# Optimization experiments

Measured on AMD Instinct MI355X. Metric: run time of the kernel, lower is better.

## Reference

```python
import jax, jax.numpy as jnp
import numpy as np

B, T, HOR, N = 64, 12, 12, 1024
DIN, DOUT, YCOV, H, K, E = 1, 1, 1, 64, 3, 8


def setup_inputs() -> dict:
    key = jax.random.key(0)
    ks = jax.random.split(key, 10)
    def g(k, shape, s=1.0):
        return jax.random.normal(k, shape, dtype=jnp.float32) * s
    # xavier-ish scale for GCN weights: 1/sqrt(fan_in)
    gi = 1.0 / np.sqrt(K * (DIN + H))
    di = 1.0 / np.sqrt(K * (DOUT + YCOV + H))
    return {
        "x": jax.random.uniform(ks[0], (B, T, N, DIN), dtype=jnp.float32),
        "y_cov": jax.random.uniform(ks[1], (B, HOR, N, YCOV), dtype=jnp.float32),
        "node_emb": g(ks[2], (N, E), 1.0),
        "enc_gate_W": g(ks[3], (K * (DIN + H), 2 * H), gi),
        "enc_gate_b": jnp.zeros((2 * H,), jnp.float32),
        "enc_upd_W": g(ks[4], (K * (DIN + H), H), gi),
        "enc_upd_b": jnp.zeros((H,), jnp.float32),
        "dec_gate_W": g(ks[5], (K * (DOUT + YCOV + H), 2 * H), di),
        "dec_gate_b": jnp.zeros((2 * H,), jnp.float32),
        "dec_upd_W": g(ks[6], (K * (DOUT + YCOV + H), H), di),
        "dec_upd_b": jnp.zeros((H,), jnp.float32),
        "proj_W": g(ks[7], (H, DOUT), 1.0 / np.sqrt(H)),
        "proj_b": jnp.zeros((DOUT,), jnp.float32),
    }


def _cheb_supports(A):
    # support_set = [I, A, 2*A@A - I, ...], cheb_k terms
    s = [jnp.eye(A.shape[0], dtype=A.dtype), A]
    for _ in range(2, K):
        s.append(2.0 * A @ s[-1] - s[-2])
    return jnp.stack(s)  # [K, N, N]


def _gcn(x, sup, W, b):
    # x: [B,N,C]; sup: [K,N,N]; matches torch cat([s_k @ x], -1) ordering (k-major)
    bb, nn, cc = x.shape
    xg = jnp.einsum('knm,bmc->bnkc', sup, x).reshape(bb, nn, K * cc)
    return xg @ W + b


def _cell(x, h, sup, gW, gb, uW, ub):
    zr = jax.nn.sigmoid(_gcn(jnp.concatenate([x, h], -1), sup, gW, gb))
    z, r = jnp.split(zr, 2, axis=-1)
    hc = jnp.tanh(_gcn(jnp.concatenate([x, z * h], -1), sup, uW, ub))
    return r * h + (1.0 - r) * hc


def reference(x, y_cov, node_emb, enc_gate_W, enc_gate_b, enc_upd_W, enc_upd_b,
              dec_gate_W, dec_gate_b, dec_upd_W, dec_upd_b, proj_W, proj_b):
    # adaptive adjacency from node embeddings (AGCRN-style)
    A = jax.nn.softmax(jax.nn.relu(node_emb @ node_emb.T), axis=-1)
    sup = _cheb_supports(A)

    h0 = jnp.zeros((B, N, H), x.dtype)

    def enc_step(h, xt):
        h2 = _cell(xt, h, sup, enc_gate_W, enc_gate_b, enc_upd_W, enc_upd_b)
        return h2, None
    h_enc, _ = jax.lax.scan(enc_step, h0, jnp.swapaxes(x, 0, 1))  # final state [B,N,H]

    go0 = jnp.zeros((B, N, DOUT), x.dtype)

    def dec_step(carry, yt):
        h, go = carry
        h2 = _cell(jnp.concatenate([go, yt], -1), h, sup,
                   dec_gate_W, dec_gate_b, dec_upd_W, dec_upd_b)
        go2 = h2 @ proj_W + proj_b
        return (h2, go2), go2
    _, outs = jax.lax.scan(dec_step, (h_enc, go0), jnp.swapaxes(y_cov, 0, 1))
    return jnp.swapaxes(outs, 0, 1)  # [B, HOR, N, DOUT]
```

## Files before the change

kernel.cpp:

```cpp
#include <hip/hip_runtime.h>
#include <math.h>

constexpr int N = 1024, B = 64, T = 12, HOR = 12, H = 64, E = 8;
constexpr size_t NBH = 4194304;

constexpr size_t A_off   = 0;
constexpr size_t Pxy_off = 1048576;
constexpr size_t h_off   = Pxy_off + 3145728;
constexpr size_t Ph_off  = h_off + NBH;
constexpr size_t zh_off  = Ph_off + 2 * NBH;
constexpr size_t r_off   = zh_off + NBH;
constexpr size_t go_off  = r_off + NBH;
constexpr size_t A2_off  = go_off + 65536;
constexpr size_t Bth_off = A2_off + 1048576;
constexpr size_t Btz_off = Bth_off + 2162688;
constexpr size_t xyK_off = Btz_off + 2097152;
constexpr size_t Pgo_off = xyK_off + 786432;
constexpr size_t wp_off  = Pgo_off + 131072;

typedef __attribute__((ext_vector_type(8))) short short8;
typedef __attribute__((ext_vector_type(4))) float f32x4;

__device__ __forceinline__ unsigned f2bf(float x) {
  unsigned u = __float_as_uint(x);
  return (u + 0x7fffu + ((u >> 16) & 1u)) >> 16;
}
__device__ __forceinline__ float bf2f(unsigned h) {
  return __uint_as_float(h << 16);
}
__device__ __forceinline__ void split4(float4 v, uint2& hi, uint2& lo) {
  unsigned h0 = f2bf(v.x), h1 = f2bf(v.y), h2 = f2bf(v.z), h3 = f2bf(v.w);
  unsigned l0 = f2bf(v.x - bf2f(h0)), l1 = f2bf(v.y - bf2f(h1));
  unsigned l2 = f2bf(v.z - bf2f(h2)), l3 = f2bf(v.w - bf2f(h3));
  hi.x = (h0 & 0xffffu) | (h1 << 16); hi.y = (h2 & 0xffffu) | (h3 << 16);
  lo.x = (l0 & 0xffffu) | (l1 << 16); lo.y = (l2 & 0xffffu) | (l3 << 16);
}

typedef const __attribute__((address_space(1))) void gas_t;
typedef __attribute__((address_space(3))) void las_t;

__global__ __launch_bounds__(256) void build_A(const float* __restrict__ emb,
                                               float* __restrict__ A) {
  __shared__ float sE[N * E];
  __shared__ float sv[N];
  __shared__ float rmax[4], rsum[4];
  const int i = blockIdx.x;
  for (int idx = threadIdx.x; idx < N * E / 4; idx += 256)
    ((float4*)sE)[idx] = ((const float4*)emb)[idx];
  __syncthreads();
  float ei[E];
#pragma unroll
  for (int e = 0; e < E; ++e) ei[e] = sE[i * E + e];
  float mymax = 0.f;
  for (int j = threadIdx.x; j < N; j += 256) {
    float d = 0.f;
#pragma unroll
    for (int e = 0; e < E; ++e) d = fmaf(ei[e], sE[j * E + e], d);
    d = fmaxf(d, 0.f);
    sv[j] = d;
    mymax = fmaxf(mymax, d);
  }
  for (int off = 32; off; off >>= 1) mymax = fmaxf(mymax, __shfl_down(mymax, off));
  const int wid = threadIdx.x >> 6, lid = threadIdx.x & 63;
  if (lid == 0) rmax[wid] = mymax;
  __syncthreads();
  const float m = fmaxf(fmaxf(rmax[0], rmax[1]), fmaxf(rmax[2], rmax[3]));
  float mysum = 0.f;
  for (int j = threadIdx.x; j < N; j += 256) {
    float ev = expf(sv[j] - m);
    sv[j] = ev;
    mysum += ev;
  }
  for (int off = 32; off; off >>= 1) mysum += __shfl_down(mysum, off);
  if (lid == 0) rsum[wid] = mysum;
  __syncthreads();
  const float inv = 1.f / (rsum[0] + rsum[1] + rsum[2] + rsum[3]);
  for (int j = threadIdx.x; j < N; j += 256) A[i * N + j] = sv[j] * inv;
}

__global__ __launch_bounds__(256) void pack_split_S(const float* __restrict__ A,
                                                    ushort* __restrict__ L,
                                                    ushort* __restrict__ R) {
  __shared__ float tile[32][33];
  const int bx = blockIdx.x * 32;
  const int by = blockIdx.y * 32;
  const int tx = threadIdx.x & 31;
  const int tg = threadIdx.x >> 5;
#pragma unroll
  for (int p = 0; p < 4; ++p) {
    int ty = tg * 4 + p;
    tile[ty][tx] = A[(size_t)(by + ty) * 1024 + bx + tx];
  }
  __syncthreads();
#pragma unroll
  for (int p = 0; p < 4; ++p) {
    int ty = tg * 4 + p;
    float v = tile[ty][tx];
    unsigned h = f2bf(v);
    unsigned l = f2bf(v - bf2f(h));
    size_t lb = (size_t)(by + ty) * 3072 + 3 * (bx + tx);
    L[lb + 0] = (ushort)h; L[lb + 1] = (ushort)l; L[lb + 2] = (ushort)h;
    float w = tile[tx][ty];
    unsigned hh = f2bf(w);
    unsigned ll = f2bf(w - bf2f(hh));
    size_t rbi = (size_t)(bx + ty) * 3072 + 3 * (by + tx);
    R[rbi + 0] = (ushort)hh; R[rbi + 1] = (ushort)hh; R[rbi + 2] = (ushort)ll;
  }
}

__global__ __launch_bounds__(256) void conv_bf16(const float* __restrict__ src,
                                                 ushort* __restrict__ dst) {
  int i = blockIdx.x * 256 + threadIdx.x;
  float4 v = ((const float4*)src)[i];
  ushort4 o;
  o.x = (ushort)f2bf(v.x); o.y = (ushort)f2bf(v.y);
  o.z = (ushort)f2bf(v.z); o.w = (ushort)f2bf(v.w);
  ((ushort4*)dst)[i] = o;
}

__global__ __launch_bounds__(256) void conv_xyK(const float* __restrict__ src,
                                                ushort* __restrict__ dst, int off) {
  int id = blockIdx.x * 256 + threadIdx.x;
  int tb = id >> 10, n = id & 1023;
  int tt = tb >> 6, b = tb & 63;
  dst[(size_t)(off + tb) * 1024 + n] = (ushort)f2bf(src[((size_t)b * T + tt) * 1024 + n]);
}

__global__ __launch_bounds__(256) void pack_W(const float* __restrict__ W,
                                              ushort* __restrict__ out,
                                              int CIN, int NC, int xoff) {
  int idx = blockIdx.x * 256 + threadIdx.x;
  int total = 3 * 2 * NC * 32;
  if (idx >= total) return;
  int kk = idx & 31;
  int colrest = idx >> 5;
  int col = colrest % NC;
  int rest = colrest / NC;
  int half = rest & 1;
  int s = rest >> 1;
  float v = W[(size_t)(s * CIN + xoff + half * 32 + kk) * NC + col];
  unsigned hi = f2bf(v);
  unsigned lo = f2bf(v - bf2f(hi));
  size_t base = (size_t)((s * 2 + half) * 2) * NC * 32;
  out[base + (size_t)col * 32 + kk] = (ushort)hi;
  out[base + (size_t)NC * 32 + (size_t)col * 32 + kk] = (ushort)lo;
}

__global__ __launch_bounds__(256) void gemm_s2p(
    const ushort* __restrict__ L, const ushort* __restrict__ R,
    float* __restrict__ P) {
  __shared__ ushort As[128 * 32];
  __shared__ ushort Bs[128 * 32];
  const int t = threadIdx.x;
  const int wave = t >> 6, lane = t & 63;
  const int bm = blockIdx.y * 128, bn = blockIdx.x * 128;
  const int wm = (wave & 1) * 64, wn = (wave >> 1) * 64;
  float* Pz = P + (size_t)blockIdx.z * 1048576;
  const int kbase = blockIdx.z * 768;

  const ushort* aSrc[2]; const ushort* bSrc[2];
  ushort* aDst[2]; ushort* bDst[2];
#pragma unroll
  for (int u = 0; u < 2; ++u) {
    int idx = wave * 128 + u * 64 + lane;
    int row = idx >> 2;
    int kq = (idx & 3) * 8;
    aSrc[u] = L + (size_t)(bm + row) * 3072 + kq;
    bSrc[u] = R + (size_t)(bn + row) * 3072 + kq;
    aDst[u] = &As[(wave * 128 + u * 64) * 8];
    bDst[u] = &Bs[(wave * 128 + u * 64) * 8];
  }
  const int lr = lane & 15;
  const int lk = (lane >> 4) * 8;
  f32x4 acc[4][4];
#pragma unroll
  for (int i = 0; i < 4; ++i)
#pragma unroll
    for (int j = 0; j < 4; ++j) acc[i][j] = {0.f, 0.f, 0.f, 0.f};

  for (int k0 = kbase; k0 < kbase + 768; k0 += 32) {
#pragma unroll
    for (int u = 0; u < 2; ++u) {
      __builtin_amdgcn_global_load_lds((gas_t*)(aSrc[u] + k0), (las_t*)aDst[u], 16, 0, 0);
      __builtin_amdgcn_global_load_lds((gas_t*)(bSrc[u] + k0), (las_t*)bDst[u], 16, 0, 0);
    }
    __syncthreads();
    short8 a[4], b[4];
#pragma unroll
    for (int i = 0; i < 4; ++i) a[i] = *(const short8*)&As[(wm + i * 16 + lr) * 32 + lk];
#pragma unroll
    for (int j = 0; j < 4; ++j) b[j] = *(const short8*)&Bs[(wn + j * 16 + lr) * 32 + lk];
#pragma unroll
    for (int i = 0; i < 4; ++i)
#pragma unroll
      for (int j = 0; j < 4; ++j)
        acc[i][j] = __builtin_amdgcn_mfma_f32_16x16x32_bf16(a[i], b[j], acc[i][j], 0, 0, 0);
    __syncthreads();
  }
  const int cr = (lane >> 4) * 4;
  const int cc = lane & 15;
#pragma unroll
  for (int i = 0; i < 4; ++i)
#pragma unroll
    for (int j = 0; j < 4; ++j) {
      int gm = bm + wm + i * 16 + cr;
      int gn = bn + wn + j * 16 + cc;
#pragma unroll
      for (int r = 0; r < 4; ++r)
        Pz[(size_t)(gm + r) * 1024 + gn] = acc[i][j][r];
    }
}

__global__ __launch_bounds__(256) void comb_s2(const float* __restrict__ P,
                                               ushort* __restrict__ A2) {
  int idx = blockIdx.x * 256 + threadIdx.x;
  float4 a = ((const float4*)P)[idx];
  float4 b = ((const float4*)(P + 1048576))[idx];
  float4 c = ((const float4*)(P + 2097152))[idx];
  float4 d = ((const float4*)(P + 3145728))[idx];
  int base = idx << 2;
  int m = base >> 10, c0 = base & 1023;
  float v0 = 2.f * (a.x + b.x + c.x + d.x) - (m == c0 + 0 ? 1.f : 0.f);
  float v1 = 2.f * (a.y + b.y + c.y + d.y) - (m == c0 + 1 ? 1.f : 0.f);
  float v2 = 2.f * (a.z + b.z + c.z + d.z) - (m == c0 + 2 ? 1.f : 0.f);
  float v3 = 2.f * (a.w + b.w + c.w + d.w) - (m == c0 + 3 ? 1.f : 0.f);
  ushort4 o;
  o.x = (ushort)f2bf(v0); o.y = (ushort)f2bf(v1);
  o.z = (ushort)f2bf(v2); o.w = (ushort)f2bf(v3);
  ((ushort4*)(A2 + 1048576))[idx] = o;
}

template <int CMODE>
__global__ __launch_bounds__(256) void gemm_bt(
    const ushort* __restrict__ A2, const ushort* __restrict__ Bt, int n1,
    float* __restrict__ C1, float* __restrict__ C2) {
  __shared__ ushort As[2][128 * 32];
  __shared__ ushort Bs[2][128 * 32];
  const int t = threadIdx.x;
  const int wave = t >> 6, lane = t & 63;
  const int bm = blockIdx.y * 128, bn = blockIdx.x * 128;
  const int wm = (wave & 1) * 64, wn = (wave >> 1) * 64;

  const ushort* aSrc[2]; const ushort* bSrc[2];
  ushort* aDst[2][2]; ushort* bDst[2][2];
#pragma unroll
  for (int u = 0; u < 2; ++u) {
    int idx = wave * 128 + u * 64 + lane;
    int row = idx >> 2;
    int kq = (idx & 3) * 8;
    aSrc[u] = A2 + (size_t)(bm + row) * 1024 + kq;
    bSrc[u] = Bt + (size_t)(bn + row) * 1024 + kq;
#pragma unroll
    for (int p = 0; p < 2; ++p) {
      aDst[p][u] = &As[p][(wave * 128 + u * 64) * 8];
      bDst[p][u] = &Bs[p][(wave * 128 + u * 64) * 8];
    }
  }
  const int lr = lane & 15, lk = (lane >> 4) * 8;
  int aOff[4], bOff[4];
#pragma unroll
  for (int i = 0; i < 4; ++i) {
    aOff[i] = (wm + i * 16 + lr) * 32 + lk;
    bOff[i] = (wn + i * 16 + lr) * 32 + lk;
  }
  f32x4 acc[4][4];
#pragma unroll
  for (int i = 0; i < 4; ++i)
#pragma unroll
    for (int j = 0; j < 4; ++j) acc[i][j] = {0.f, 0.f, 0.f, 0.f};

  for (int k0 = 0; k0 < 1024; k0 += 64) {
#pragma unroll
    for (int p = 0; p < 2; ++p)
#pragma unroll
      for (int u = 0; u < 2; ++u) {
        __builtin_amdgcn_global_load_lds((gas_t*)(aSrc[u] + k0 + p * 32),
                                         (las_t*)aDst[p][u], 16, 0, 0);
        __builtin_amdgcn_global_load_lds((gas_t*)(bSrc[u] + k0 + p * 32),
                                         (las_t*)bDst[p][u], 16, 0, 0);
      }
    __syncthreads();
#pragma unroll
    for (int p = 0; p < 2; ++p) {
      short8 a[4], b[4];
#pragma unroll
      for (int i = 0; i < 4; ++i) a[i] = *(const short8*)&As[p][aOff[i]];
#pragma unroll
      for (int j = 0; j < 4; ++j) b[j] = *(const short8*)&Bs[p][bOff[j]];
#pragma unroll
      for (int i = 0; i < 4; ++i)
#pragma unroll
        for (int j = 0; j < 4; ++j)
          acc[i][j] = __builtin_amdgcn_mfma_f32_16x16x32_bf16(a[i], b[j], acc[i][j], 0, 0, 0);
    }
    __syncthreads();
  }

  const int cr = (lane >> 4) * 4;
  const int cc = lane & 15;
#pragma unroll
  for (int i = 0; i < 4; ++i) {
#pragma unroll
    for (int j = 0; j < 4; ++j) {
      int gm = bm + wm + i * 16 + cr;
      int gn = bn + wn + j * 16 + cc;
      if (gn < n1) {
        if (CMODE == 0) {
          float* p = C1 + (size_t)gm * n1 + gn;
#pragma unroll
          for (int r = 0; r < 4; ++r) p[(size_t)r * n1] = acc[i][j][r];
        } else {
          int half = gm >> 10, nn = gm & 1023;
          float* p = C1 + (size_t)half * NBH +
                     ((size_t)(gn >> 6) * 1024 + nn) * 64 + (gn & 63);
#pragma unroll
          for (int r = 0; r < 4; ++r) p[(size_t)r * 64] = acc[i][j][r];
        }
      } else if (C2 != nullptr && gn < n1 + 64) {
        float* p = C2 + (size_t)gm * 64 + (gn - n1);
#pragma unroll
        for (int r = 0; r < 4; ++r) p[(size_t)r * 64] = acc[i][j][r];
      }
    }
  }
}

template <int NX>
__global__ __launch_bounds__(256, 4) void gate_mfma(
    const float* __restrict__ hmat, const float* __restrict__ Ph,
    const ushort* __restrict__ Wp, const float* __restrict__ Wf, const float* __restrict__ bias,
    const float* __restrict__ xb0, int xbs0, const float* __restrict__ xp0, int xs0,
    const float* __restrict__ xb1, int xbs1, const float* __restrict__ xp1, int xs1,
    float* __restrict__ zh, float* __restrict__ rbuf, ushort* __restrict__ Btz) {
  constexpr int CIN = NX + 64;
  __shared__ ushort smem[12288];
  ushort* Ah = smem;
  ushort* Al = smem + 2048;
  ushort* Bh = smem + 4096;
  ushort* Bl = smem + 8192;
  ushort* transT = smem;
  __shared__ float sxv[3][2][64];
  __shared__ float sWx[3][2][128];
  const int t = threadIdx.x;
  const int wave = t >> 6, lane = t & 63;
  const int bm = blockIdx.x * 64;
  const int wm = (wave & 1) * 32, wn = (wave >> 1) * 64;
  const int lr = lane & 15, lk = (lane >> 4) * 8;
  const float* srcs[3] = {hmat, Ph, Ph + NBH};

  if (t < 64) {
    int grow = bm + t;
    int n = grow & 1023, b = grow >> 10;
    sxv[0][0][t] = xb0[(size_t)b * xbs0 + n];
    sxv[1][0][t] = xp0[(size_t)n * xs0 + b];
    sxv[2][0][t] = xp0[(size_t)1024 * xs0 + (size_t)n * xs0 + b];
    if (NX == 2) {
      sxv[0][1][t] = xb1[(size_t)b * xbs1 + n];
      sxv[1][1][t] = xp1[(size_t)n * xs1 + b];
      sxv[2][1][t] = xp1[(size_t)1024 * xs1 + (size_t)n * xs1 + b];
    }
  } else if (t < 192) {
    int col = t - 64;
#pragma unroll
    for (int s = 0; s < 3; ++s)
#pragma unroll
      for (int f = 0; f < NX; ++f)
        sWx[s][f][col] = Wf[(size_t)(s * CIN + f) * 128 + col];
  }

  int arow[2], ajq[2];
#pragma unroll
  for (int p = 0; p < 2; ++p) {
    int f = p * 256 + t;
    arow[p] = f >> 3;
    ajq[p] = (f & 7) * 4;
  }
  float4 pf[2];
#pragma unroll
  for (int p = 0; p < 2; ++p)
    pf[p] = *(const float4*)(hmat + (size_t)(bm + arow[p]) * 64 + ajq[p]);

  f32x4 acc[2][4];
#pragma unroll
  for (int i = 0; i < 2; ++i)
#pragma unroll
    for (int j = 0; j < 4; ++j) acc[i][j] = {0.f, 0.f, 0.f, 0.f};

  for (int it = 0; it < 6; ++it) {
    const int s = it >> 1, half = it & 1;
#pragma unroll
    for (int p = 0; p < 2; ++p) {
      uint2 hi, lo;
      split4(pf[p], hi, lo);
      *(uint2*)&Ah[arow[p] * 32 + ajq[p]] = hi;
      *(uint2*)&Al[arow[p] * 32 + ajq[p]] = lo;
    }
    const ushort* wph = Wp + (size_t)((s * 2 + half) * 2) * (128 * 32);
    const ushort* wpl = wph + 128 * 32;
#pragma unroll
    for (int u = 0; u < 2; ++u) {
      int idx = wave * 128 + u * 64 + lane;
      __builtin_amdgcn_global_load_lds((gas_t*)(wph + idx * 8), (las_t*)&Bh[idx * 8], 16, 0, 0);
      __builtin_amdgcn_global_load_lds((gas_t*)(wpl + idx * 8), (las_t*)&Bl[idx * 8], 16, 0, 0);
    }
    __syncthreads();
    if (it < 5) {
      const float* nsrc = srcs[(it + 1) >> 1];
      const int nj0 = ((it + 1) & 1) * 32;
#pragma unroll
      for (int p = 0; p < 2; ++p)
        pf[p] = *(const float4*)(nsrc + (size_t)(bm + arow[p]) * 64 + nj0 + ajq[p]);
    }
    short8 ah[2], al[2], bh[4], bl[4];
#pragma unroll
    for (int i = 0; i < 2; ++i) {
      ah[i] = *(const short8*)&Ah[(wm + i * 16 + lr) * 32 + lk];
      al[i] = *(const short8*)&Al[(wm + i * 16 + lr) * 32 + lk];
    }
#pragma unroll
    for (int j = 0; j < 4; ++j) {
      bh[j] = *(const short8*)&Bh[(wn + j * 16 + lr) * 32 + lk];
      bl[j] = *(const short8*)&Bl[(wn + j * 16 + lr) * 32 + lk];
    }
#pragma unroll
    for (int i = 0; i < 2; ++i)
#pragma unroll
      for (int j = 0; j < 4; ++j) {
        acc[i][j] = __builtin_amdgcn_mfma_f32_16x16x32_bf16(ah[i], bh[j], acc[i][j], 0, 0, 0);
        acc[i][j] = __builtin_amdgcn_mfma_f32_16x16x32_bf16(al[i], bh[j], acc[i][j], 0, 0, 0);
        acc[i][j] = __builtin_amdgcn_mfma_f32_16x16x32_bf16(ah[i], bl[j], acc[i][j], 0, 0, 0);
      }
    __syncthreads();
  }

  const int cr = (lane >> 4) * 4;
  const int cc = lane & 15;
#pragma unroll
  for (int i = 0; i < 2; ++i) {
#pragma unroll
    for (int j = 0; j < 4; ++j) {
      int col = wn + j * 16 + cc;
      float bcol = bias[col];
#pragma unroll
      for (int r = 0; r < 4; ++r) {
        int rowl = wm + i * 16 + cr + r;
        int grow = bm + rowl;
        float v = acc[i][j][r] + bcol;
#pragma unroll
        for (int s = 0; s < 3; ++s)
#pragma unroll
          for (int f = 0; f < NX; ++f)
            v = fmaf(sxv[s][f][rowl], sWx[s][f][col], v);
        float sig = 1.f / (1.f + expf(-v));
        if (col < 64) {
          float zv = sig * hmat[(size_t)grow * 64 + col];
          zh[(size_t)grow * 64 + col] = zv;
          transT[col * 72 + rowl] = (ushort)f2bf(zv);
        } else {
          rbuf[(size_t)grow * 64 + col - 64] = sig;
        }
      }
    }
  }
  __syncthreads();
  const int bq = bm >> 10, nb = bm & 1023;
  for (int idx = t; idx < 512; idx += 256) {
    int j = idx >> 3, ch = idx & 7;
    uint4 v = *(const uint4*)&transT[j * 72 + ch * 8];
    *(uint4*)(Btz + (((size_t)(bq * 64 + j)) << 10) + nb + ch * 8) = v;
  }
}

template <int NX, int PROJ>
__global__ __launch_bounds__(256, 4) void upd_mfma(
    float* __restrict__ hmat, const float* __restrict__ zhb, const float* __restrict__ Pzh,
    const ushort* __restrict__ Wp, const float* __restrict__ Wf, const float* __restrict__ bias,
    const float* __restrict__ xb0, int xbs0, const float* __restrict__ xp0, int xs0,
    const float* __restrict__ xb1, int xbs1, const float* __restrict__ xp1, int xs1,
    const float* __restrict__ rbuf, ushort* __restrict__ Bth,
    const float* __restrict__ pW, const float* __restrict__ pb,
    float* __restrict__ gobuf, float* __restrict__ outp, int tstep) {
  constexpr int CIN = NX + 64;
  __shared__ ushort smem[8192];
  ushort* Ah = smem;
  ushort* Al = smem + 2048;
  ushort* Bh = smem + 4096;
  ushort* Bl = smem + 6144;
  ushort* transT = smem;
  __shared__ float sxv[3][2][64];
  __shared__ float sWx[3][2][64];
  __shared__ float part[2][64];
  const int t = threadIdx.x;
  const int wave = t >> 6, lane = t & 63;
  const int bm = blockIdx.x * 64;
  const int wm = (wave & 1) * 32, wn = (wave >> 1) * 32;
  const int lr = lane & 15, lk = (lane >> 4) * 8;
  const float* srcs[3] = {zhb, Pzh, Pzh + NBH};

  if (t < 64) {
    int grow = bm + t;
    int n = grow & 1023, b = grow >> 10;
    sxv[0][0][t] = xb0[(size_t)b * xbs0 + n];
    sxv[1][0][t] = xp0[(size_t)n * xs0 + b];
    sxv[2][0][t] = xp0[(size_t)1024 * xs0 + (size_t)n * xs0 + b];
    if (NX == 2) {
      sxv[0][1][t] = xb1[(size_t)b * xbs1 + n];
      sxv[1][1][t] = xp1[(size_t)n * xs1 + b];
      sxv[2][1][t] = xp1[(size_t)1024 * xs1 + (size_t)n * xs1 + b];
    }
  } else if (t < 128) {
    int col = t - 64;
#pragma unroll
    for (int s = 0; s < 3; ++s)
#pragma unroll
      for (int f = 0; f < NX; ++f)
        sWx[s][f][col] = Wf[(size_t)(s * CIN + f) * 64 + col];
  }

  int arow[2], ajq[2];
#pragma unroll
  for (int p = 0; p < 2; ++p) {
    int f = p * 256 + t;
    arow[p] = f >> 3;
    ajq[p] = (f & 7) * 4;
  }
  float4 pf[2];
#pragma unroll
  for (int p = 0; p < 2; ++p)
    pf[p] = *(const float4*)(zhb + (size_t)(bm + arow[p]) * 64 + ajq[p]);

  f32x4 acc[2][2];
#pragma unroll
  for (int i = 0; i < 2; ++i)
#pragma unroll
    for (int j = 0; j < 2; ++j) acc[i][j] = {0.f, 0.f, 0.f, 0.f};

  for (int it = 0; it < 6; ++it) {
    const int s = it >> 1, half = it & 1;
#pragma unroll
    for (int p = 0; p < 2; ++p) {
      uint2 hi, lo;
      split4(pf[p], hi, lo);
      *(uint2*)&Ah[arow[p] * 32 + ajq[p]] = hi;
      *(uint2*)&Al[arow[p] * 32 + ajq[p]] = lo;
    }
    const ushort* wph = Wp + (size_t)((s * 2 + half) * 2) * (64 * 32);
    const ushort* wpl = wph + 64 * 32;
    {
      int idx = wave * 64 + lane;
      __builtin_amdgcn_global_load_lds((gas_t*)(wph + idx * 8), (las_t*)&Bh[idx * 8], 16, 0, 0);
      __builtin_amdgcn_global_load_lds((gas_t*)(wpl + idx * 8), (las_t*)&Bl[idx * 8], 16, 0, 0);
    }
    __syncthreads();
    if (it < 5) {
      const float* nsrc = srcs[(it + 1) >> 1];
      const int nj0 = ((it + 1) & 1) * 32;
#pragma unroll
      for (int p = 0; p < 2; ++p)
        pf[p] = *(const float4*)(nsrc + (size_t)(bm + arow[p]) * 64 + nj0 + ajq[p]);
    }
    short8 ah[2], al[2], bh[2], bl[2];
#pragma unroll
    for (int i = 0; i < 2; ++i) {
      ah[i] = *(const short8*)&Ah[(wm + i * 16 + lr) * 32 + lk];
      al[i] = *(const short8*)&Al[(wm + i * 16 + lr) * 32 + lk];
    }
#pragma unroll
    for (int j = 0; j < 2; ++j) {
      bh[j] = *(const short8*)&Bh[(wn + j * 16 + lr) * 32 + lk];
      bl[j] = *(const short8*)&Bl[(wn + j * 16 + lr) * 32 + lk];
    }
#pragma unroll
    for (int i = 0; i < 2; ++i)
#pragma unroll
      for (int j = 0; j < 2; ++j) {
        acc[i][j] = __builtin_amdgcn_mfma_f32_16x16x32_bf16(ah[i], bh[j], acc[i][j], 0, 0, 0);
        acc[i][j] = __builtin_amdgcn_mfma_f32_16x16x32_bf16(al[i], bh[j], acc[i][j], 0, 0, 0);
        acc[i][j] = __builtin_amdgcn_mfma_f32_16x16x32_bf16(ah[i], bl[j], acc[i][j], 0, 0, 0);
      }
    __syncthreads();
  }

  const int cr = (lane >> 4) * 4;
  const int cc = lane & 15;
  float psv[2][4];
#pragma unroll
  for (int i = 0; i < 2; ++i)
#pragma unroll
    for (int r = 0; r < 4; ++r) psv[i][r] = 0.f;

#pragma unroll
  for (int i = 0; i < 2; ++i) {
#pragma unroll
    for (int j = 0; j < 2; ++j) {
      int col = wn + j * 16 + cc;
      float bcol = bias[col];
      float pwc = PROJ ? pW[col] : 0.f;
#pragma unroll
      for (int r = 0; r < 4; ++r) {
        int rowl = wm + i * 16 + cr + r;
        int grow = bm + rowl;
        float v = acc[i][j][r] + bcol;
#pragma unroll
        for (int s = 0; s < 3; ++s)
#pragma unroll
          for (int f = 0; f < NX; ++f)
            v = fmaf(sxv[s][f][rowl], sWx[s][f][col], v);
        float hc = tanhf(v);
        size_t idx = (size_t)grow * 64 + col;
        float rr = rbuf[idx];
        float ho = hmat[idx];
        float o = rr * ho + (1.f - rr) * hc;
        hmat[idx] = o;
        transT[col * 72 + rowl] = (ushort)f2bf(o);
        if (PROJ) psv[i][r] += o * pwc;
      }
    }
  }
  if (PROJ) {
#pragma unroll
    for (int i = 0; i < 2; ++i)
#pragma unroll
      for (int r = 0; r < 4; ++r)
#pragma unroll
        for (int off = 8; off; off >>= 1)
          psv[i][r] += __shfl_down(psv[i][r], off, 16);
    if (cc == 0) {
#pragma unroll
      for (int i = 0; i < 2; ++i)
#pragma unroll
        for (int r = 0; r < 4; ++r)
          part[wn >> 5][wm + i * 16 + cr + r] = psv[i][r];
    }
  }
  __syncthreads();
  const int bq = bm >> 10, nb = bm & 1023;
  for (int idx = t; idx < 512; idx += 256) {
    int j = idx >> 3, ch = idx & 7;
    uint4 v = *(const uint4*)&transT[j * 72 + ch * 8];
    *(uint4*)(Bth + (((size_t)(bq * 64 + j)) << 10) + nb + ch * 8) = v;
  }
  if (PROJ && t < 64) {
    int grow = bm + t;
    int n = grow & 1023, b = grow >> 10;
    float g = part[0][t] + part[1][t] + pb[0];
    gobuf[grow] = g;
    outp[((size_t)b * HOR + tstep) * N + n] = g;
    Bth[((size_t)(4096 + b)) * 1024 + n] = (ushort)f2bf(g);
  }
}

extern "C" void kernel_launch(void* const* d_in, const int* in_sizes, int n_in,
                              void* d_out, int out_size, void* d_ws, size_t ws_size,
                              hipStream_t stream) {
  const float* x    = (const float*)d_in[0];
  const float* ycov = (const float*)d_in[1];
  const float* emb  = (const float*)d_in[2];
  const float* egW  = (const float*)d_in[3];
  const float* egb  = (const float*)d_in[4];
  const float* euW  = (const float*)d_in[5];
  const float* eub  = (const float*)d_in[6];
  const float* dgW  = (const float*)d_in[7];
  const float* dgb  = (const float*)d_in[8];
  const float* duW  = (const float*)d_in[9];
  const float* dub  = (const float*)d_in[10];
  const float* pW   = (const float*)d_in[11];
  const float* pb   = (const float*)d_in[12];
  float* out = (float*)d_out;
  float* ws  = (float*)d_ws;

  float* Amat = ws + A_off;
  float* Pxy  = ws + Pxy_off;
  float* hmat = ws + h_off;
  float* Ph   = ws + Ph_off;
  float* zh   = ws + zh_off;
  float* rb   = ws + r_off;
  float* gob  = ws + go_off;
  float* Pgo  = ws + Pgo_off;
  ushort* A2   = (ushort*)(ws + A2_off);
  ushort* Bth  = (ushort*)(ws + Bth_off);
  ushort* Btz  = (ushort*)(ws + Btz_off);
  ushort* xyK  = (ushort*)(ws + xyK_off);
  ushort* AspL = (ushort*)(ws + zh_off);
  ushort* AspR = (ushort*)(ws + r_off);
  float*  Pp   = ws + Ph_off;
  ushort* WPge = (ushort*)(ws + wp_off);
  ushort* WPgd = WPge + 2 * 24576;
  ushort* WPue = WPgd + 2 * 24576;
  ushort* WPud = WPue + 2 * 12288;

  build_A<<<N, 256, 0, stream>>>(emb, Amat);
  pack_split_S<<<dim3(32, 32), 256, 0, stream>>>(Amat, AspL, AspR);
  gemm_s2p<<<dim3(8, 8, 4), 256, 0, stream>>>(AspL, AspR, Pp);
  comb_s2<<<1024, 256, 0, stream>>>(Pp, A2);
  conv_bf16<<<1024, 256, 0, stream>>>(Amat, A2);
  conv_xyK<<<3072, 256, 0, stream>>>(x, xyK, 0);
  conv_xyK<<<3072, 256, 0, stream>>>(ycov, xyK, 768);
  pack_W<<<(3 * 2 * 128 * 32 + 255) / 256, 256, 0, stream>>>(egW, WPge, 65, 128, 1);
  pack_W<<<(3 * 2 * 128 * 32 + 255) / 256, 256, 0, stream>>>(dgW, WPgd, 66, 128, 2);
  pack_W<<<(3 * 2 * 64 * 32 + 255) / 256, 256, 0, stream>>>(euW, WPue, 65, 64, 1);
  pack_W<<<(3 * 2 * 64 * 32 + 255) / 256, 256, 0, stream>>>(duW, WPud, 66, 64, 2);
  gemm_bt<0><<<dim3(12, 16), 256, 0, stream>>>(A2, xyK, 1536, Pxy, nullptr);
  (void)hipMemsetAsync(hmat, 0, NBH * sizeof(float), stream);
  (void)hipMemsetAsync(Ph, 0, 2 * NBH * sizeof(float), stream);
  (void)hipMemsetAsync(gob, 0, 65536 * sizeof(float), stream);
  (void)hipMemsetAsync(Bth + (size_t)4096 * 1024, 0, 128 * 1024 * sizeof(ushort), stream);

  for (int t = 0; t < T; ++t) {
    if (t > 0)
      gemm_bt<1><<<dim3(32, 16), 256, 0, stream>>>(A2, Bth, 4096, Ph, nullptr);
    gate_mfma<1><<<1024, 256, 0, stream>>>(hmat, Ph, WPge, egW, egb,
                                           x + t * 1024, T * 1024, Pxy + t * 64, 1536,
                                           nullptr, 0, nullptr, 0, zh, rb, Btz);
    if (t > 0)
      gemm_bt<1><<<dim3(32, 16), 256, 0, stream>>>(A2, Btz, 4096, Ph, nullptr);
    upd_mfma<1, 0><<<1024, 256, 0, stream>>>(hmat, zh, Ph, WPue, euW, eub,
                                             x + t * 1024, T * 1024, Pxy + t * 64, 1536,
                                             nullptr, 0, nullptr, 0, rb, Bth,
                                             nullptr, nullptr, nullptr, nullptr, 0);
  }

  for (int t = 0; t < HOR; ++t) {
    gemm_bt<1><<<dim3(33, 16), 256, 0, stream>>>(A2, Bth, 4096, Ph, Pgo);
    gate_mfma<2><<<1024, 256, 0, stream>>>(hmat, Ph, WPgd, dgW, dgb,
                                           gob, 1024, Pgo, 64,
                                           ycov + t * 1024, HOR * 1024,
                                           Pxy + 768 + t * 64, 1536, zh, rb, Btz);
    gemm_bt<1><<<dim3(32, 16), 256, 0, stream>>>(A2, Btz, 4096, Ph, nullptr);
    upd_mfma<2, 1><<<1024, 256, 0, stream>>>(hmat, zh, Ph, WPud, duW, dub,
                                             gob, 1024, Pgo, 64,
                                             ycov + t * 1024, HOR * 1024,
                                             Pxy + 768 + t * 64, 1536,
                                             rb, Bth, pW, pb, gob, out, t);
  }
}
```

Baseline: 2.701 ms.

## Store graph-propagated hidden states in fp16 and use single fp16 MFMA

The support-times-hidden GEMM now writes its outputs (Ph) as fp16 instead of fp32. The gate and update kernels consume them with one fp16 MFMA per tile instead of the bf16 hi/lo split, which needed three MFMAs plus on-the-fly splitting. The identity term (hmat/zh) keeps the split-bf16 path, and weights for supports 1-2 are packed separately into fp16. This halves traffic for the largest intermediate buffers and cuts MFMA work. The gemm_bt grid is also flattened and remapped into grouped tiles for better L2 locality, at the cost of some precision on the propagated terms.

```diff
diff --git a/kernel.cpp b/kernel.cpp
--- a/kernel.cpp
+++ b/kernel.cpp
@@ -19,6 +19,7 @@
 constexpr size_t wp_off  = Pgo_off + 131072;
 
 typedef __attribute__((ext_vector_type(8))) short short8;
+typedef _Float16 half8 __attribute__((ext_vector_type(8)));
 typedef __attribute__((ext_vector_type(4))) float f32x4;
 
 __device__ __forceinline__ unsigned f2bf(float x) {
@@ -27,6 +28,12 @@
 }
 __device__ __forceinline__ float bf2f(unsigned h) {
   return __uint_as_float(h << 16);
+}
+__device__ __forceinline__ ushort f2h(float x) {
+  _Float16 h = (_Float16)x;
+  ushort u;
+  __builtin_memcpy(&u, &h, 2);
+  return u;
 }
 __device__ __forceinline__ void split4(float4 v, uint2& hi, uint2& lo) {
   unsigned h0 = f2bf(v.x), h1 = f2bf(v.y), h2 = f2bf(v.z), h3 = f2bf(v.w);
@@ -126,24 +133,39 @@
   dst[(size_t)(off + tb) * 1024 + n] = (ushort)f2bf(src[((size_t)b * T + tt) * 1024 + n]);
 }
 
-__global__ __launch_bounds__(256) void pack_W(const float* __restrict__ W,
-                                              ushort* __restrict__ out,
-                                              int CIN, int NC, int xoff) {
+__global__ __launch_bounds__(256) void pack_Wbf(const float* __restrict__ W,
+                                                ushort* __restrict__ out,
+                                                int CIN, int NC, int xoff) {
   int idx = blockIdx.x * 256 + threadIdx.x;
-  int total = 3 * 2 * NC * 32;
+  int total = 2 * NC * 32;
   if (idx >= total) return;
   int kk = idx & 31;
-  int colrest = idx >> 5;
-  int col = colrest % NC;
-  int rest = colrest / NC;
-  int half = rest & 1;
-  int s = rest >> 1;
-  float v = W[(size_t)(s * CIN + xoff + half * 32 + kk) * NC + col];
+  int rest = idx >> 5;
+  int col = rest % NC;
+  int half = rest / NC;
+  float v = W[(size_t)(xoff + half * 32 + kk) * NC + col];
   unsigned hi = f2bf(v);
   unsigned lo = f2bf(v - bf2f(hi));
-  size_t base = (size_t)((s * 2 + half) * 2) * NC * 32;
+  size_t base = (size_t)(half * 2) * NC * 32;
   out[base + (size_t)col * 32 + kk] = (ushort)hi;
   out[base + (size_t)NC * 32 + (size_t)col * 32 + kk] = (ushort)lo;
+}
+
+__global__ __launch_bounds__(256) void pack_W16(const float* __restrict__ W,
+                                                ushort* __restrict__ out,
+                                                int CIN, int NC, int xoff) {
+  int idx = blockIdx.x * 256 + threadIdx.x;
+  int total = 2 * 2 * NC * 32;
+  if (idx >= total) return;
+  int kk = idx & 31;
+  int rest = idx >> 5;
+  int col = rest % NC;
+  rest /= NC;
+  int half = rest & 1;
+  int s1 = rest >> 1;
+  int s = s1 + 1;
+  float v = W[(size_t)(s * CIN + xoff + half * 32 + kk) * NC + col];
+  out[(size_t)(s1 * 2 + half) * NC * 32 + (size_t)col * 32 + kk] = f2h(v);
 }
 
 __global__ __launch_bounds__(256) void gemm_s2p(
@@ -233,12 +255,24 @@
 template <int CMODE>
 __global__ __launch_bounds__(256) void gemm_bt(
     const ushort* __restrict__ A2, const ushort* __restrict__ Bt, int n1,
-    float* __restrict__ C1, float* __restrict__ C2) {
+    ushort* __restrict__ C1h, float* __restrict__ C1f, float* __restrict__ C2) {
   __shared__ ushort As[2][128 * 32];
   __shared__ ushort Bs[2][128 * 32];
   const int t = threadIdx.x;
   const int wave = t >> 6, lane = t & 63;
-  const int bm = blockIdx.y * 128, bn = blockIdx.x * 128;
+  int bxi, byi;
+  if (CMODE == 0) {
+    bxi = blockIdx.x; byi = blockIdx.y;
+  } else {
+    int lin = blockIdx.x;
+    if (lin < 512) {
+      bxi = (lin & 7) * 4 + ((lin >> 3) & 3);
+      byi = lin >> 5;
+    } else {
+      bxi = 32; byi = lin - 512;
+    }
+  }
+  const int bm = byi * 128, bn = bxi * 128;
   const int wm = (wave & 1) * 64, wn = (wave >> 1) * 64;
 
   const ushort* aSrc[2]; const ushort* bSrc[2];
@@ -306,15 +340,15 @@
       int gn = bn + wn + j * 16 + cc;
       if (gn < n1) {
         if (CMODE == 0) {
-          float* p = C1 + (size_t)gm * n1 + gn;
+          float* p = C1f + (size_t)gm * n1 + gn;
 #pragma unroll
           for (int r = 0; r < 4; ++r) p[(size_t)r * n1] = acc[i][j][r];
         } else {
           int half = gm >> 10, nn = gm & 1023;
-          float* p = C1 + (size_t)half * NBH +
-                     ((size_t)(gn >> 6) * 1024 + nn) * 64 + (gn & 63);
-#pragma unroll
-          for (int r = 0; r < 4; ++r) p[(size_t)r * 64] = acc[i][j][r];
+          ushort* p = C1h + (size_t)half * NBH +
+                      ((size_t)(gn >> 6) * 1024 + nn) * 64 + (gn & 63);
+#pragma unroll
+          for (int r = 0; r < 4; ++r) p[(size_t)r * 64] = f2h(acc[i][j][r]);
         }
       } else if (C2 != nullptr && gn < n1 + 64) {
         float* p = C2 + (size_t)gm * 64 + (gn - n1);
@@ -327,8 +361,9 @@
 
 template <int NX>
 __global__ __launch_bounds__(256, 4) void gate_mfma(
-    const float* __restrict__ hmat, const float* __restrict__ Ph,
-    const ushort* __restrict__ Wp, const float* __restrict__ Wf, const float* __restrict__ bias,
+    const float* __restrict__ hmat, const ushort* __restrict__ Ph16,
+    const ushort* __restrict__ Wbf, const ushort* __restrict__ W16,
+    const float* __restrict__ Wf, const float* __restrict__ bias,
     const float* __restrict__ xb0, int xbs0, const float* __restrict__ xp0, int xs0,
     const float* __restrict__ xb1, int xbs1, const float* __restrict__ xp1, int xs1,
     float* __restrict__ zh, float* __restrict__ rbuf, ushort* __restrict__ Btz) {
@@ -338,6 +373,8 @@
   ushort* Al = smem + 2048;
   ushort* Bh = smem + 4096;
   ushort* Bl = smem + 8192;
+  ushort* A16 = smem;
+  ushort* B16 = smem + 4096;
   ushort* transT = smem;
   __shared__ float sxv[3][2][64];
   __shared__ float sWx[3][2][128];
@@ -346,7 +383,6 @@
   const int bm = blockIdx.x * 64;
   const int wm = (wave & 1) * 32, wn = (wave >> 1) * 64;
   const int lr = lane & 15, lk = (lane >> 4) * 8;
-  const float* srcs[3] = {hmat, Ph, Ph + NBH};
 
   if (t < 64) {
     int grow = bm + t;
@@ -375,10 +411,13 @@
     arow[p] = f >> 3;
     ajq[p] = (f & 7) * 4;
   }
+  const int hrow = t >> 2, hjq = (t & 3) * 8;
+
   float4 pf[2];
 #pragma unroll
   for (int p = 0; p < 2; ++p)
     pf[p] = *(const float4*)(hmat + (size_t)(bm + arow[p]) * 64 + ajq[p]);
+  uint4 px;
 
   f32x4 acc[2][4];
 #pragma unroll
@@ -386,8 +425,8 @@
 #pragma unroll
     for (int j = 0; j < 4; ++j) acc[i][j] = {0.f, 0.f, 0.f, 0.f};
 
-  for (int it = 0; it < 6; ++it) {
-    const int s = it >> 1, half = it & 1;
+#pragma unroll
+  for (int half = 0; half < 2; ++half) {
 #pragma unroll
     for (int p = 0; p < 2; ++p) {
       uint2 hi, lo;
@@ -395,7 +434,7 @@
       *(uint2*)&Ah[arow[p] * 32 + ajq[p]] = hi;
       *(uint2*)&Al[arow[p] * 32 + ajq[p]] = lo;
     }
-    const ushort* wph = Wp + (size_t)((s * 2 + half) * 2) * (128 * 32);
+    const ushort* wph = Wbf + (size_t)(half * 2) * (128 * 32);
     const ushort* wpl = wph + 128 * 32;
 #pragma unroll
     for (int u = 0; u < 2; ++u) {
@@ -404,12 +443,12 @@
       __builtin_amdgcn_global_load_lds((gas_t*)(wpl + idx * 8), (las_t*)&Bl[idx * 8], 16, 0, 0);
     }
     __syncthreads();
-    if (it < 5) {
-      const float* nsrc = srcs[(it + 1) >> 1];
-      const int nj0 = ((it + 1) & 1) * 32;
+    if (half == 0) {
 #pragma unroll
       for (int p = 0; p < 2; ++p)
-        pf[p] = *(const float4*)(nsrc + (size_t)(bm + arow[p]) * 64 + nj0 + ajq[p]);
+        pf[p] = *(const float4*)(hmat + (size_t)(bm + arow[p]) * 64 + 32 + ajq[p]);
+    } else {
+      px = *(const uint4*)(Ph16 + (size_t)(bm + hrow) * 64 + hjq);
     }
     short8 ah[2], al[2], bh[4], bl[4];
 #pragma unroll
@@ -430,6 +469,36 @@
         acc[i][j] = __builtin_amdgcn_mfma_f32_16x16x32_bf16(al[i], bh[j], acc[i][j], 0, 0, 0);
         acc[i][j] = __builtin_amdgcn_mfma_f32_16x16x32_bf16(ah[i], bl[j], acc[i][j], 0, 0, 0);
       }
+    __syncthreads();
+  }
+
+  for (int it = 0; it < 4; ++it) {
+    const int s1 = it >> 1, half = it & 1;
+    *(uint4*)&A16[hrow * 32 + hjq] = px;
+    const ushort* w16 = W16 + (size_t)(s1 * 2 + half) * (128 * 32);
+#pragma unroll
+    for (int u = 0; u < 2; ++u) {
+      int idx = wave * 128 + u * 64 + lane;
+      __builtin_amdgcn_global_load_lds((gas_t*)(w16 + idx * 8), (las_t*)&B16[idx * 8], 16, 0, 0);
+    }
+    __syncthreads();
+    if (it < 3) {
+      const int nit = it + 1;
+      const ushort* src = Ph16 + (size_t)(nit >> 1) * NBH;
+      px = *(const uint4*)(src + (size_t)(bm + hrow) * 64 + (nit & 1) * 32 + hjq);
+    }
+    half8 a16[2], b16[4];
+#pragma unroll
+    for (int i = 0; i < 2; ++i)
+      a16[i] = *(const half8*)&A16[(wm + i * 16 + lr) * 32 + lk];
+#pragma unroll
+    for (int j = 0; j < 4; ++j)
+      b16[j] = *(const half8*)&B16[(wn + j * 16 + lr) * 32 + lk];
+#pragma unroll
+    for (int i = 0; i < 2; ++i)
+#pragma unroll
+      for (int j = 0; j < 4; ++j)
+        acc[i][j] = __builtin_amdgcn_mfma_f32_16x16x32_f16(a16[i], b16[j], acc[i][j], 0, 0, 0);
     __syncthreads();
   }
 
@@ -473,8 +542,9 @@
 
 template <int NX, int PROJ>
 __global__ __launch_bounds__(256, 4) void upd_mfma(
-    float* __restrict__ hmat, const float* __restrict__ zhb, const float* __restrict__ Pzh,
-    const ushort* __restrict__ Wp, const float* __restrict__ Wf, const float* __restrict__ bias,
+    float* __restrict__ hmat, const float* __restrict__ zhb, const ushort* __restrict__ Pzh16,
+    const ushort* __restrict__ Wbf, const ushort* __restrict__ W16,
+    const float* __restrict__ Wf, const float* __restrict__ bias,
     const float* __restrict__ xb0, int xbs0, const float* __restrict__ xp0, int xs0,
     const float* __restrict__ xb1, int xbs1, const float* __restrict__ xp1, int xs1,
     const float* __restrict__ rbuf, ushort* __restrict__ Bth,
@@ -486,6 +556,8 @@
   ushort* Al = smem + 2048;
   ushort* Bh = smem + 4096;
   ushort* Bl = smem + 6144;
+  ushort* A16 = smem;
+  ushort* B16 = smem + 4096;
   ushort* transT = smem;
   __shared__ float sxv[3][2][64];
   __shared__ float sWx[3][2][64];
@@ -495,7 +567,6 @@
   const int bm = blockIdx.x * 64;
   const int wm = (wave & 1) * 32, wn = (wave >> 1) * 32;
   const int lr = lane & 15, lk = (lane >> 4) * 8;
-  const float* srcs[3] = {zhb, Pzh, Pzh + NBH};
 
   if (t < 64) {
     int grow = bm + t;
@@ -524,10 +595,13 @@
     arow[p] = f >> 3;
     ajq[p] = (f & 7) * 4;
   }
+  const int hrow = t >> 2, hjq = (t & 3) * 8;
+
   float4 pf[2];
 #pragma unroll
   for (int p = 0; p < 2; ++p)
     pf[p] = *(const float4*)(zhb + (size_t)(bm + arow[p]) * 64 + ajq[p]);
+  uint4 px;
 
   f32x4 acc[2][2];
 #pragma unroll
@@ -535,8 +609,8 @@
 #pragma unroll
     for (int j = 0; j < 2; ++j) acc[i][j] = {0.f, 0.f, 0.f, 0.f};
 
-  for (int it = 0; it < 6; ++it) {
-    const int s = it >> 1, half = it & 1;
+#pragma unroll
+  for (int half = 0; half < 2; ++half) {
 #pragma unroll
     for (int p = 0; p < 2; ++p) {
       uint2 hi, lo;
@@ -544,7 +618,7 @@
       *(uint2*)&Ah[arow[p] * 32 + ajq[p]] = hi;
       *(uint2*)&Al[arow[p] * 32 + ajq[p]] = lo;
     }
-    const ushort* wph = Wp + (size_t)((s * 2 + half) * 2) * (64 * 32);
+    const ushort* wph = Wbf + (size_t)(half * 2) * (64 * 32);
     const ushort* wpl = wph + 64 * 32;
     {
       int idx = wave * 64 + lane;
@@ -552,12 +626,12 @@
       __builtin_amdgcn_global_load_lds((gas_t*)(wpl + idx * 8), (las_t*)&Bl[idx * 8], 16, 0, 0);
     }
     __syncthreads();
-    if (it < 5) {
-      const float* nsrc = srcs[(it + 1) >> 1];
-      const int nj0 = ((it + 1) & 1) * 32;
+    if (half == 0) {
 #pragma unroll
       for (int p = 0; p < 2; ++p)
-        pf[p] = *(const float4*)(nsrc + (size_t)(bm + arow[p]) * 64 + nj0 + ajq[p]);
+        pf[p] = *(const float4*)(zhb + (size_t)(bm + arow[p]) * 64 + 32 + ajq[p]);
+    } else {
+      px = *(const uint4*)(Pzh16 + (size_t)(bm + hrow) * 64 + hjq);
     }
     short8 ah[2], al[2], bh[2], bl[2];
 #pragma unroll
@@ -578,6 +652,35 @@
         acc[i][j] = __builtin_amdgcn_mfma_f32_16x16x32_bf16(al[i], bh[j], acc[i][j], 0, 0, 0);
         acc[i][j] = __builtin_amdgcn_mfma_f32_16x16x32_bf16(ah[i], bl[j], acc[i][j], 0, 0, 0);
       }
+    __syncthreads();
+  }
+
+  for (int it = 0; it < 4; ++it) {
+    const int s1 = it >> 1, half = it & 1;
+    *(uint4*)&A16[hrow * 32 + hjq] = px;
+    const ushort* w16 = W16 + (size_t)(s1 * 2 + half) * (64 * 32);
+    {
+      int idx = wave * 64 + lane;
+      __builtin_amdgcn_global_load_lds((gas_t*)(w16 + idx * 8), (las_t*)&B16[idx * 8], 16, 0, 0);
+    }
+    __syncthreads();
+    if (it < 3) {
+      const int nit = it + 1;
+      const ushort* src = Pzh16 + (size_t)(nit >> 1) * NBH;
+      px = *(const uint4*)(src + (size_t)(bm + hrow) * 64 + (nit & 1) * 32 + hjq);
+    }
+    half8 a16[2], b16[2];
+#pragma unroll
+    for (int i = 0; i < 2; ++i)
+      a16[i] = *(const half8*)&A16[(wm + i * 16 + lr) * 32 + lk];
+#pragma unroll
+    for (int j = 0; j < 2; ++j)
+      b16[j] = *(const half8*)&B16[(wn + j * 16 + lr) * 32 + lk];
+#pragma unroll
+    for (int i = 0; i < 2; ++i)
+#pragma unroll
+      for (int j = 0; j < 2; ++j)
+        acc[i][j] = __builtin_amdgcn_mfma_f32_16x16x32_f16(a16[i], b16[j], acc[i][j], 0, 0, 0);
     __syncthreads();
   }
 
@@ -672,7 +775,7 @@
   float* Amat = ws + A_off;
   float* Pxy  = ws + Pxy_off;
   float* hmat = ws + h_off;
-  float* Ph   = ws + Ph_off;
+  ushort* Ph16 = (ushort*)(ws + Ph_off);
   float* zh   = ws + zh_off;
   float* rb   = ws + r_off;
   float* gob  = ws + go_off;
@@ -684,10 +787,15 @@
   ushort* AspL = (ushort*)(ws + zh_off);
   ushort* AspR = (ushort*)(ws + r_off);
   float*  Pp   = ws + Ph_off;
-  ushort* WPge = (ushort*)(ws + wp_off);
-  ushort* WPgd = WPge + 2 * 24576;
-  ushort* WPue = WPgd + 2 * 24576;
-  ushort* WPud = WPue + 2 * 12288;
+  ushort* WB   = (ushort*)(ws + wp_off);
+  ushort* WbfGE = WB;
+  ushort* WbfGD = WB + 16384;
+  ushort* WbfUE = WB + 32768;
+  ushort* WbfUD = WB + 40960;
+  ushort* W16GE = WB + 49152;
+  ushort* W16GD = WB + 65536;
+  ushort* W16UE = WB + 81920;
+  ushort* W16UD = WB + 90112;
 
   build_A<<<N, 256, 0, stream>>>(emb, Amat);
   pack_split_S<<<dim3(32, 32), 256, 0, stream>>>(Amat, AspL, AspR);
@@ -696,38 +804,42 @@
   conv_bf16<<<1024, 256, 0, stream>>>(Amat, A2);
   conv_xyK<<<3072, 256, 0, stream>>>(x, xyK, 0);
   conv_xyK<<<3072, 256, 0, stream>>>(ycov, xyK, 768);
-  pack_W<<<(3 * 2 * 128 * 32 + 255) / 256, 256, 0, stream>>>(egW, WPge, 65, 128, 1);
-  pack_W<<<(3 * 2 * 128 * 32 + 255) / 256, 256, 0, stream>>>(dgW, WPgd, 66, 128, 2);
-  pack_W<<<(3 * 2 * 64 * 32 + 255) / 256, 256, 0, stream>>>(euW, WPue, 65, 64, 1);
-  pack_W<<<(3 * 2 * 64 * 32 + 255) / 256, 256, 0, stream>>>(duW, WPud, 66, 64, 2);
-  gemm_bt<0><<<dim3(12, 16), 256, 0, stream>>>(A2, xyK, 1536, Pxy, nullptr);
+  pack_Wbf<<<32, 256, 0, stream>>>(egW, WbfGE, 65, 128, 1);
+  pack_Wbf<<<32, 256, 0, stream>>>(dgW, WbfGD, 66, 128, 2);
+  pack_Wbf<<<16, 256, 0, stream>>>(euW, WbfUE, 65, 64, 1);
+  pack_Wbf<<<16, 256, 0, stream>>>(duW, WbfUD, 66, 64, 2);
+  pack_W16<<<64, 256, 0, stream>>>(egW, W16GE, 65, 128, 1);
+  pack_W16<<<64, 256, 0, stream>>>(dgW, W16GD, 66, 128, 2);
+  pack_W16<<<32, 256, 0, stream>>>(euW, W16UE, 65, 64, 1);
+  pack_W16<<<32, 256, 0, stream>>>(duW, W16UD, 66, 64, 2);
+  gemm_bt<0><<<dim3(12, 16), 256, 0, stream>>>(A2, xyK, 1536, nullptr, Pxy, nullptr);
   (void)hipMemsetAsync(hmat, 0, NBH * sizeof(float), stream);
-  (void)hipMemsetAsync(Ph, 0, 2 * NBH * sizeof(float), stream);
+  (void)hipMemsetAsync(Ph16, 0, 2 * NBH * sizeof(ushort), stream);
   (void)hipMemsetAsync(gob, 0, 65536 * sizeof(float), stream);
   (void)hipMemsetAsync(Bth + (size_t)4096 * 1024, 0, 128 * 1024 * sizeof(ushort), stream);
 
   for (int t = 0; t < T; ++t) {
     if (t > 0)
-      gemm_bt<1><<<dim3(32, 16), 256, 0, stream>>>(A2, Bth, 4096, Ph, nullptr);
-    gate_mfma<1><<<1024, 256, 0, stream>>>(hmat, Ph, WPge, egW, egb,
+      gemm_bt<1><<<512, 256, 0, stream>>>(A2, Bth, 4096, Ph16, nullptr, nullptr);
+    gate_mfma<1><<<1024, 256, 0, stream>>>(hmat, Ph16, WbfGE, W16GE, egW, egb,
                                            x + t * 1024, T * 1024, Pxy + t * 64, 1536,
                                            nullptr, 0, nullptr, 0, zh, rb, Btz);
     if (t > 0)
-      gemm_bt<1><<<dim3(32, 16), 256, 0, stream>>>(A2, Btz, 4096, Ph, nullptr);
-    upd_mfma<1, 0><<<1024, 256, 0, stream>>>(hmat, zh, Ph, WPue, euW, eub,
+      gemm_bt<1><<<512, 256, 0, stream>>>(A2, Btz, 4096, Ph16, nullptr, nullptr);
+    upd_mfma<1, 0><<<1024, 256, 0, stream>>>(hmat, zh, Ph16, WbfUE, W16UE, euW, eub,
                                              x + t * 1024, T * 1024, Pxy + t * 64, 1536,
                                              nullptr, 0, nullptr, 0, rb, Bth,
                                              nullptr, nullptr, nullptr, nullptr, 0);
   }
 
   for (int t = 0; t < HOR; ++t) {
-    gemm_bt<1><<<dim3(33, 16), 256, 0, stream>>>(A2, Bth, 4096, Ph, Pgo);
-    gate_mfma<2><<<1024, 256, 0, stream>>>(hmat, Ph, WPgd, dgW, dgb,
+    gemm_bt<1><<<528, 256, 0, stream>>>(A2, Bth, 4096, Ph16, nullptr, Pgo);
+    gate_mfma<2><<<1024, 256, 0, stream>>>(hmat, Ph16, WbfGD, W16GD, dgW, dgb,
                                            gob, 1024, Pgo, 64,
                                            ycov + t * 1024, HOR * 1024,
                                            Pxy + 768 + t * 64, 1536, zh, rb, Btz);
-    gemm_bt<1><<<dim3(32, 16), 256, 0, stream>>>(A2, Btz, 4096, Ph, nullptr);
-    upd_mfma<2, 1><<<1024, 256, 0, stream>>>(hmat, zh, Ph, WPud, duW, dub,
+    gemm_bt<1><<<512, 256, 0, stream>>>(A2, Btz, 4096, Ph16, nullptr, nullptr);
+    upd_mfma<2, 1><<<1024, 256, 0, stream>>>(hmat, zh, Ph16, WbfUD, W16UD, duW, dub,
                                              gob, 1024, Pgo, 64,
                                              ycov + t * 1024, HOR * 1024,
                                              Pxy + 768 + t * 64, 1536,
```

Result: faster. 2.504 ms, median of 2 (-7.3%).
